# Kernel tuning notes

Hardware: AMD Instinct MI355X
Metric: run time of the kernel (lower is better)

## Reference

```python
import jax, jax.numpy as jnp
import numpy as np

N_EMBD = 1024
N_HEAD = 16
BLOCK_SIZE = 2048
B, T = 4, 2048


def setup_inputs() -> dict:
    key = jax.random.key(0)
    ks = jax.random.split(key, 5)
    x = jax.random.normal(ks[0], (B, T, N_EMBD), dtype=jnp.float32)
    s_in = 1.0 / np.sqrt(N_EMBD)
    W_attn = jax.random.normal(ks[1], (N_EMBD, 3 * N_EMBD), dtype=jnp.float32) * s_in
    b_attn = jnp.zeros((3 * N_EMBD,), dtype=jnp.float32)
    W_proj = jax.random.normal(ks[2], (N_EMBD, N_EMBD), dtype=jnp.float32) * s_in
    b_proj = jnp.zeros((N_EMBD,), dtype=jnp.float32)
    return {"x": x, "W_attn": W_attn, "b_attn": b_attn, "W_proj": W_proj, "b_proj": b_proj}


def reference(x, W_attn, b_attn, W_proj, b_proj):
    Bb, Tt, C = x.shape
    hd = C // N_HEAD  # head_dim = 64
    qkv = x @ W_attn + b_attn                       # [B,T,3C]
    q, k, v = jnp.split(qkv, 3, axis=-1)
    q = q.reshape(Bb, Tt, N_HEAD, hd).transpose(0, 2, 1, 3)  # [B,H,T,hd]
    k = k.reshape(Bb, Tt, N_HEAD, hd).transpose(0, 2, 1, 3)
    v = v.reshape(Bb, Tt, N_HEAD, hd).transpose(0, 2, 1, 3)
    scores = jnp.einsum('bhqd,bhkd->bhqk', q, k) / jnp.sqrt(jnp.float32(hd))
    causal = jnp.tril(jnp.ones((Tt, Tt), dtype=bool))[None, None]
    scores = jnp.where(causal, scores, -jnp.inf)
    attn = jax.nn.softmax(scores, axis=-1)          # [B,H,T,T]
    y = jnp.einsum('bhqk,bhkd->bhqd', attn, v)      # [B,H,T,hd]
    y = y.transpose(0, 2, 1, 3).reshape(Bb, Tt, C)
    return y @ W_proj + b_proj
```

## Files before the change

kernel.cpp:

```cpp
#include <hip/hip_runtime.h>

#define N_EMBD 1024
#define N_HEAD 16
#define HD 64
#define BSZ 4
#define TSEQ 2048
#define MROWS (BSZ * TSEQ)

using bf16x8 = __attribute__((ext_vector_type(8))) short;
using f32x4  = __attribute__((ext_vector_type(4))) float;

__device__ __forceinline__ ushort f2bf(float f) {
    uint u = __float_as_uint(f);
    u += 0x7FFFu + ((u >> 16) & 1u);
    return (ushort)(u >> 16);
}
__device__ __forceinline__ float bf2f(ushort h) {
    return __uint_as_float(((uint)h) << 16);
}

__device__ __forceinline__ void gload16(const ushort* g, short* l) {
    __builtin_amdgcn_global_load_lds(
        (const __attribute__((address_space(1))) void*)g,
        (__attribute__((address_space(3))) void*)l, 16, 0, 0);
}

__global__ __launch_bounds__(256) void split_bf16(const float* __restrict__ A,
                                                  ushort* __restrict__ H,
                                                  ushort* __restrict__ L)
{
    const size_t i = ((size_t)blockIdx.x * 256 + threadIdx.x) * 4;
    const float4 v = *(const float4*)&A[i];
    ushort4 h, l;
    h.x = f2bf(v.x); l.x = f2bf(v.x - bf2f(h.x));
    h.y = f2bf(v.y); l.y = f2bf(v.y - bf2f(h.y));
    h.z = f2bf(v.z); l.z = f2bf(v.z - bf2f(h.z));
    h.w = f2bf(v.w); l.w = f2bf(v.w - bf2f(h.w));
    *(ushort4*)&H[i] = h;
    *(ushort4*)&L[i] = l;
}

__global__ __launch_bounds__(256) void transpose_split(
    const float* __restrict__ W, ushort* __restrict__ Th, ushort* __restrict__ Tl,
    int K, int N)
{
    __shared__ float t[32][33];
    const int k0 = blockIdx.y * 32;
    const int n0 = blockIdx.x * 32;
    const int c = threadIdx.x & 31;
    const int r = threadIdx.x >> 5;
    #pragma unroll
    for (int i = 0; i < 4; ++i)
        t[r + i * 8][c] = W[(size_t)(k0 + r + i * 8) * N + n0 + c];
    __syncthreads();
    #pragma unroll
    for (int i = 0; i < 4; ++i) {
        const float v = t[c][r + i * 8];
        const ushort hb = f2bf(v);
        const ushort lb = f2bf(v - bf2f(hb));
        const size_t o = (size_t)(n0 + r + i * 8) * K + k0 + c;
        Th[o] = hb;
        Tl[o] = lb;
    }
}

__global__ __launch_bounds__(256) void transpose_v(
    const ushort* __restrict__ qkvh, ushort* __restrict__ vth)
{
    __shared__ __align__(16) ushort tr[64][72];
    const int t0 = blockIdx.x * 64;
    const int h  = blockIdx.y;
    const int b  = blockIdx.z;
    const int r  = threadIdx.x >> 2;
    const int c4 = (threadIdx.x & 3) * 16;

    const size_t inb = ((size_t)(b * TSEQ + t0 + r)) * (3 * N_EMBD) + 2 * N_EMBD + h * HD + c4;
    *(float4*)&tr[r][c4]     = *(const float4*)&qkvh[inb];
    *(float4*)&tr[r][c4 + 8] = *(const float4*)&qkvh[inb + 8];
    __syncthreads();

    ushort v[16] __attribute__((aligned(16)));
    #pragma unroll
    for (int u = 0; u < 16; ++u) v[u] = tr[c4 + u][r];
    const size_t ob = (((size_t)(b * N_HEAD + h)) * HD + r) * TSEQ + t0 + c4;
    *(float4*)&vth[ob]     = ((const float4*)v)[0];
    *(float4*)&vth[ob + 8] = ((const float4*)v)[1];
}

template<bool ASPLIT, bool OUTBF16>
__global__ __launch_bounds__(256) void gemm_mfma(
    const ushort* __restrict__ Ah, const ushort* __restrict__ Al,
    const ushort* __restrict__ Bh, const ushort* __restrict__ Bl,
    const float* __restrict__ bias,
    float* __restrict__ Cf, ushort* __restrict__ Ch, ushort* __restrict__ Cl,
    int M, int N, int K)
{
    __shared__ __align__(16) short lds_raw[16384];

    const int tid  = threadIdx.x;
    const int wave = tid >> 6;
    const int lane = tid & 63;
    const int wr   = wave >> 1;
    const int wc   = wave & 1;
    const int row0 = blockIdx.y * 128;
    const int col0 = blockIdx.x * 128;

    const int sr  = wave * 32 + (lane >> 2);
    const int sco = (lane & 3) * 8;
    const ushort* gAh = Ah + (size_t)(row0 + sr) * K + sco;
    const ushort* gAl = ASPLIT ? (Al + (size_t)(row0 + sr) * K + sco) : nullptr;
    const ushort* gBh = Bh + (size_t)(col0 + sr) * K + sco;
    const ushort* gBl = Bl + (size_t)(col0 + sr) * K + sco;
    short* const ldst = lds_raw + wave * 1024;

    const int fr = lane & 15;
    const int fq = lane >> 4;
    const int ko = fq * 8;

    f32x4 acc[4][4] = {};

    for (int k0 = 0; k0 < K; k0 += 32) {
        const size_t K16 = (size_t)16 * K;
        gload16(gAh + k0,       ldst);
        gload16(gAh + k0 + K16, ldst + 512);
        if (ASPLIT) {
            gload16(gAl + k0,       ldst + 4096);
            gload16(gAl + k0 + K16, ldst + 4096 + 512);
        }
        gload16(gBh + k0,       ldst + 8192);
        gload16(gBh + k0 + K16, ldst + 8192 + 512);
        gload16(gBl + k0,       ldst + 12288);
        gload16(gBl + k0 + K16, ldst + 12288 + 512);
        __syncthreads();

        bf16x8 a_h[4], a_l[4], b_h[4], b_l[4];
        #pragma unroll
        for (int m = 0; m < 4; ++m) {
            const int r = wr * 64 + m * 16 + fr;
            a_h[m] = *(const bf16x8*)&lds_raw[r * 32 + ko];
            if (ASPLIT) a_l[m] = *(const bf16x8*)&lds_raw[4096 + r * 32 + ko];
        }
        #pragma unroll
        for (int n = 0; n < 4; ++n) {
            const int r = wc * 64 + n * 16 + fr;
            b_h[n] = *(const bf16x8*)&lds_raw[8192 + r * 32 + ko];
            b_l[n] = *(const bf16x8*)&lds_raw[12288 + r * 32 + ko];
        }

        #pragma unroll
        for (int m = 0; m < 4; ++m)
            #pragma unroll
            for (int n = 0; n < 4; ++n) {
                acc[m][n] = __builtin_amdgcn_mfma_f32_16x16x32_bf16(a_h[m], b_h[n], acc[m][n], 0, 0, 0);
                if (ASPLIT)
                    acc[m][n] = __builtin_amdgcn_mfma_f32_16x16x32_bf16(a_l[m], b_h[n], acc[m][n], 0, 0, 0);
                acc[m][n] = __builtin_amdgcn_mfma_f32_16x16x32_bf16(a_h[m], b_l[n], acc[m][n], 0, 0, 0);
            }
        __syncthreads();
    }

    float bv[4];
    #pragma unroll
    for (int n = 0; n < 4; ++n) bv[n] = bias[col0 + wc * 64 + n * 16 + fr];

    if (OUTBF16) {
        short* wbuf = lds_raw + wave * 2048;
        #pragma unroll
        for (int t = 0; t < 2; ++t) {
            ushort* dst = (t == 0) ? Ch : Cl;
            #pragma unroll
            for (int half = 0; half < 2; ++half) {
                __syncthreads();
                #pragma unroll
                for (int m2 = 0; m2 < 2; ++m2) {
                    const int m = half * 2 + m2;
                    #pragma unroll
                    for (int j = 0; j < 4; ++j)
                        #pragma unroll
                        for (int n = 0; n < 4; ++n) {
                            const float o = acc[m][n][j] + bv[n];
                            const ushort hb = f2bf(o);
                            wbuf[(m2 * 16 + fq * 4 + j) * 64 + n * 16 + fr] =
                                (short)(t == 0 ? hb : f2bf(o - bf2f(hb)));
                        }
                }
                __syncthreads();
                #pragma unroll
                for (int i = 0; i < 4; ++i) {
                    const int r = i * 8 + (lane >> 3);
                    const bf16x8 v = *(const bf16x8*)&wbuf[r * 64 + (lane & 7) * 8];
                    *(bf16x8*)&dst[(size_t)(row0 + wr * 64 + half * 32 + r) * N
                                   + col0 + wc * 64 + (lane & 7) * 8] = v;
                }
            }
        }
    } else {
        float* fbuf = (float*)lds_raw + wave * 2048;
        #pragma unroll
        for (int half = 0; half < 2; ++half) {
            __syncthreads();
            #pragma unroll
            for (int m2 = 0; m2 < 2; ++m2) {
                const int m = half * 2 + m2;
                #pragma unroll
                for (int j = 0; j < 4; ++j)
                    #pragma unroll
                    for (int n = 0; n < 4; ++n)
                        fbuf[(m2 * 16 + fq * 4 + j) * 64 + n * 16 + fr] = acc[m][n][j] + bv[n];
            }
            __syncthreads();
            #pragma unroll
            for (int i = 0; i < 8; ++i) {
                const int r = i * 4 + (lane >> 4);
                const float4 v = *(const float4*)&fbuf[r * 64 + (lane & 15) * 4];
                *(float4*)&Cf[(size_t)(row0 + wr * 64 + half * 32 + r) * N
                              + col0 + wc * 64 + (lane & 15) * 4] = v;
            }
        }
    }
}

__global__ __launch_bounds__(512, 4) void flash_attn_mfma(
    const ushort* __restrict__ qkvh, const ushort* __restrict__ qkvl,
    const ushort* __restrict__ vth, ushort* __restrict__ ath)
{
    __shared__ __align__(16) short Kh[64][64];
    __shared__ __align__(16) short Kl[64][64];
    __shared__ __align__(16) short Vs[64][64];
    __shared__ __align__(16) short Pw[8][2][16][72];

    const int tid  = threadIdx.x;
    const int wave = tid >> 6;
    const int lane = tid & 63;
    const int fr = lane & 15;
    const int g  = lane >> 4;
    const int q0 = blockIdx.x * 128;
    const int h  = blockIdx.y;
    const int b  = blockIdx.z;
    const int qw = q0 + wave * 16;
    const int qg = qw + fr;

    const size_t qrow = ((size_t)(b * TSEQ + qg)) * (3 * N_EMBD) + h * HD + 8 * g;
    const bf16x8 qh0 = *(const bf16x8*)&qkvh[qrow];
    const bf16x8 qh1 = *(const bf16x8*)&qkvh[qrow + 32];
    const bf16x8 ql0 = *(const bf16x8*)&qkvl[qrow];
    const bf16x8 ql1 = *(const bf16x8*)&qkvl[qrow + 32];

    f32x4 O[4] = {};
    float mrun = -1e30f, lrun = 0.f;

    const int sr  = tid >> 3;
    const int su  = tid & 7;
    const int spu = (su ^ (sr & 7)) * 8;
    const int sc  = su * 8;
    const ushort* kgh = qkvh + ((size_t)(b * TSEQ + sr)) * (3 * N_EMBD) + N_EMBD + h * HD + sc;
    const ushort* kgl = qkvl + ((size_t)(b * TSEQ + sr)) * (3 * N_EMBD) + N_EMBD + h * HD + sc;
    const ushort* vg  = vth + (((size_t)(b * N_HEAD + h)) * HD + sr) * TSEQ + sc;

    const int x7  = fr & 7;
    const int ru0 = (g ^ x7) * 8;
    const int ru1 = ((4 + g) ^ x7) * 8;

    const int nt = q0 / 64 + 2;

    float4 nkh = *(const float4*)(kgh);
    float4 nkl = *(const float4*)(kgl);
    float4 nv  = *(const float4*)(vg);

    for (int kt = 0; kt < nt; ++kt) {
        __syncthreads();
        *(float4*)&Kh[sr][spu] = nkh;
        *(float4*)&Kl[sr][spu] = nkl;
        *(float4*)&Vs[sr][spu] = nv;
        __syncthreads();

        if (kt + 1 < nt) {
            nkh = *(const float4*)(kgh + (size_t)(kt + 1) * 64 * 3 * N_EMBD);
            nkl = *(const float4*)(kgl + (size_t)(kt + 1) * 64 * 3 * N_EMBD);
            nv  = *(const float4*)(vg + (kt + 1) * 64);
        }

        if (kt * 64 > qw + 15) continue;

        f32x4 s[4] = {};
        __builtin_amdgcn_s_setprio(1);
        #pragma unroll
        for (int kf = 0; kf < 4; ++kf) {
            const int kr = kf * 16 + fr;
            const bf16x8 kh0 = *(const bf16x8*)&Kh[kr][ru0];
            const bf16x8 kl0 = *(const bf16x8*)&Kl[kr][ru0];
            const bf16x8 kh1 = *(const bf16x8*)&Kh[kr][ru1];
            const bf16x8 kl1 = *(const bf16x8*)&Kl[kr][ru1];
            s[kf] = __builtin_amdgcn_mfma_f32_16x16x32_bf16(kh0, qh0, s[kf], 0, 0, 0);
            s[kf] = __builtin_amdgcn_mfma_f32_16x16x32_bf16(kl0, qh0, s[kf], 0, 0, 0);
            s[kf] = __builtin_amdgcn_mfma_f32_16x16x32_bf16(kh0, ql0, s[kf], 0, 0, 0);
            s[kf] = __builtin_amdgcn_mfma_f32_16x16x32_bf16(kh1, qh1, s[kf], 0, 0, 0);
            s[kf] = __builtin_amdgcn_mfma_f32_16x16x32_bf16(kl1, qh1, s[kf], 0, 0, 0);
            s[kf] = __builtin_amdgcn_mfma_f32_16x16x32_bf16(kh1, ql1, s[kf], 0, 0, 0);
        }
        __builtin_amdgcn_s_setprio(0);

        const bool dm = (kt * 64 + 63 > qw);
        float tmax = -1e30f;
        #pragma unroll
        for (int kf = 0; kf < 4; ++kf)
            #pragma unroll
            for (int j = 0; j < 4; ++j) {
                float v = s[kf][j] * 0.125f;
                if (dm && (kt * 64 + kf * 16 + 4 * g + j > qg)) v = -1e30f;
                s[kf][j] = v;
                tmax = fmaxf(tmax, v);
            }
        tmax = fmaxf(tmax, __shfl_xor(tmax, 16));
        tmax = fmaxf(tmax, __shfl_xor(tmax, 32));
        const float mn = fmaxf(mrun, tmax);
        const float sf = __expf(mrun - mn);
        mrun = mn;
        lrun *= sf;
        #pragma unroll
        for (int df = 0; df < 4; ++df)
            #pragma unroll
            for (int j = 0; j < 4; ++j) O[df][j] *= sf;

        #pragma unroll
        for (int kf = 0; kf < 4; ++kf) {
            uint hw0, hw1, lw0, lw1;
            {
                const float p0 = __expf(s[kf][0] - mn);
                const float p1 = __expf(s[kf][1] - mn);
                const float p2 = __expf(s[kf][2] - mn);
                const float p3 = __expf(s[kf][3] - mn);
                const ushort h0 = f2bf(p0), h1 = f2bf(p1), h2 = f2bf(p2), h3 = f2bf(p3);
                const ushort l0 = f2bf(p0 - bf2f(h0)), l1 = f2bf(p1 - bf2f(h1));
                const ushort l2 = f2bf(p2 - bf2f(h2)), l3 = f2bf(p3 - bf2f(h3));
                lrun += (bf2f(h0) + bf2f(l0)) + (bf2f(h1) + bf2f(l1))
                      + (bf2f(h2) + bf2f(l2)) + (bf2f(h3) + bf2f(l3));
                hw0 = (uint)h0 | ((uint)h1 << 16);
                hw1 = (uint)h2 | ((uint)h3 << 16);
                lw0 = (uint)l0 | ((uint)l1 << 16);
                lw1 = (uint)l2 | ((uint)l3 << 16);
            }
            const int kb = kf * 16 + 4 * g;
            *(uint*)&Pw[wave][0][fr][kb]     = hw0;
            *(uint*)&Pw[wave][0][fr][kb + 2] = hw1;
            *(uint*)&Pw[wave][1][fr][kb]     = lw0;
            *(uint*)&Pw[wave][1][fr][kb + 2] = lw1;
        }

        #pragma unroll
        for (int c = 0; c < 2; ++c) {
            const bf16x8 pbh = *(const bf16x8*)&Pw[wave][0][fr][c * 32 + 8 * g];
            const bf16x8 pbl = *(const bf16x8*)&Pw[wave][1][fr][c * 32 + 8 * g];
            const int rvc = ((4 * c + g) ^ x7) * 8;
            __builtin_amdgcn_s_setprio(1);
            #pragma unroll
            for (int df = 0; df < 4; ++df) {
                const bf16x8 va = *(const bf16x8*)&Vs[df * 16 + fr][rvc];
                O[df] = __builtin_amdgcn_mfma_f32_16x16x32_bf16(va, pbh, O[df], 0, 0, 0);
                O[df] = __builtin_amdgcn_mfma_f32_16x16x32_bf16(va, pbl, O[df], 0, 0, 0);
            }
            __builtin_amdgcn_s_setprio(0);
        }
    }

    lrun += __shfl_xor(lrun, 16);
    lrun += __shfl_xor(lrun, 32);
    const float inv = 1.f / lrun;

    float* Ol = (float*)&Pw[wave][0][0][0];
    #pragma unroll
    for (int df = 0; df < 4; ++df)
        #pragma unroll
        for (int j = 0; j < 4; ++j)
            Ol[fr * 68 + df * 16 + 4 * g + j] = O[df][j] * inv;

    const int q2 = lane >> 2;
    const int dl = (lane & 3) * 4;
    const size_t orow = ((size_t)(b * TSEQ + q0 + wave * 16 + q2)) * N_EMBD + h * HD;
    #pragma unroll
    for (int i = 0; i < 4; ++i) {
        const float4 y = *(const float4*)&Ol[q2 * 68 + dl + 16 * i];
        ushort4 o4;
        o4.x = f2bf(y.x); o4.y = f2bf(y.y); o4.z = f2bf(y.z); o4.w = f2bf(y.w);
        *(ushort4*)&ath[orow + dl + 16 * i] = o4;
    }
}

extern "C" void kernel_launch(void* const* d_in, const int* in_sizes, int n_in,
                              void* d_out, int out_size, void* d_ws, size_t ws_size,
                              hipStream_t stream) {
    const float* x      = (const float*)d_in[0];
    const float* W_attn = (const float*)d_in[1];
    const float* b_attn = (const float*)d_in[2];
    const float* W_proj = (const float*)d_in[3];
    const float* b_proj = (const float*)d_in[4];
    float* out = (float*)d_out;
    (void)in_sizes; (void)n_in; (void)out_size; (void)ws_size;

    char* ws = (char*)d_ws;
    ushort* qkvh = (ushort*)ws; ws += (size_t)MROWS * 3 * N_EMBD * 2;
    ushort* qkvl = (ushort*)ws; ws += (size_t)MROWS * 3 * N_EMBD * 2;
    ushort* xh   = (ushort*)ws; ws += (size_t)MROWS * N_EMBD * 2;
    ushort* xl   = (ushort*)ws; ws += (size_t)MROWS * N_EMBD * 2;
    ushort* wah  = (ushort*)ws; ws += (size_t)3 * N_EMBD * N_EMBD * 2;
    ushort* wal  = (ushort*)ws; ws += (size_t)3 * N_EMBD * N_EMBD * 2;
    ushort* wph  = (ushort*)ws; ws += (size_t)N_EMBD * N_EMBD * 2;
    ushort* wpl  = (ushort*)ws; ws += (size_t)N_EMBD * N_EMBD * 2;
    ushort* vth  = (ushort*)ws; ws += (size_t)MROWS * N_EMBD * 2;
    ushort* ath  = (ushort*)ws;

    dim3 blk(256);

    split_bf16<<<dim3(MROWS * N_EMBD / 1024), blk, 0, stream>>>(x, xh, xl);
    transpose_split<<<dim3(3 * N_EMBD / 32, N_EMBD / 32), blk, 0, stream>>>(
        W_attn, wah, wal, N_EMBD, 3 * N_EMBD);
    transpose_split<<<dim3(N_EMBD / 32, N_EMBD / 32), blk, 0, stream>>>(
        W_proj, wph, wpl, N_EMBD, N_EMBD);

    gemm_mfma<true, true><<<dim3(3 * N_EMBD / 128, MROWS / 128), blk, 0, stream>>>(
        xh, xl, wah, wal, b_attn, nullptr, qkvh, qkvl, MROWS, 3 * N_EMBD, N_EMBD);

    transpose_v<<<dim3(TSEQ / 64, N_HEAD, BSZ), blk, 0, stream>>>(qkvh, vth);

    flash_attn_mfma<<<dim3(TSEQ / 128, N_HEAD, BSZ), dim3(512), 0, stream>>>(
        qkvh, qkvl, vth, ath);

    gemm_mfma<false, false><<<dim3(N_EMBD / 128, MROWS / 128), blk, 0, stream>>>(
        ath, nullptr, wph, wpl, b_proj, out, nullptr, nullptr, MROWS, N_EMBD, N_EMBD);
}
```

Before: 515.8 us.

## Fold softmax scale into Q weights, use exp2, lazy rescale, and swizzle blocks

```diff
diff --git a/kernel.cpp b/kernel.cpp
--- a/kernel.cpp
+++ b/kernel.cpp
@@ -7,6 +7,8 @@
 #define TSEQ 2048
 #define MROWS (BSZ * TSEQ)
 
+#define QSCALE 0.1803368801111204f
+
 using bf16x8 = __attribute__((ext_vector_type(8))) short;
 using f32x4  = __attribute__((ext_vector_type(4))) float;
 
@@ -17,6 +19,13 @@
 }
 __device__ __forceinline__ float bf2f(ushort h) {
     return __uint_as_float(((uint)h) << 16);
+}
+__device__ __forceinline__ float fexp2(float x) {
+#if __has_builtin(__builtin_amdgcn_exp2f)
+    return __builtin_amdgcn_exp2f(x);
+#else
+    return exp2f(x);
+#endif
 }
 
 __device__ __forceinline__ void gload16(const ushort* g, short* l) {
@@ -42,7 +51,7 @@
 
 __global__ __launch_bounds__(256) void transpose_split(
     const float* __restrict__ W, ushort* __restrict__ Th, ushort* __restrict__ Tl,
-    int K, int N)
+    int K, int N, int scaled_rows, float rowscale)
 {
     __shared__ float t[32][33];
     const int k0 = blockIdx.y * 32;
@@ -55,10 +64,12 @@
     __syncthreads();
     #pragma unroll
     for (int i = 0; i < 4; ++i) {
-        const float v = t[c][r + i * 8];
+        const int n = n0 + r + i * 8;
+        float v = t[c][r + i * 8];
+        if (n < scaled_rows) v *= rowscale;
         const ushort hb = f2bf(v);
         const ushort lb = f2bf(v - bf2f(hb));
-        const size_t o = (size_t)(n0 + r + i * 8) * K + k0 + c;
+        const size_t o = (size_t)n * K + k0 + c;
         Th[o] = hb;
         Tl[o] = lb;
     }
@@ -93,17 +104,23 @@
     const ushort* __restrict__ Bh, const ushort* __restrict__ Bl,
     const float* __restrict__ bias,
     float* __restrict__ Cf, ushort* __restrict__ Ch, ushort* __restrict__ Cl,
-    int M, int N, int K)
+    int M, int N, int K, int qcols)
 {
     __shared__ __align__(16) short lds_raw[16384];
+
+    const uint flat = blockIdx.y * gridDim.x + blockIdx.x;
+    const uint nwg  = gridDim.x * gridDim.y;
+    const uint swz  = (flat & 7) * (nwg >> 3) + (flat >> 3);
+    const int  bx   = swz % gridDim.x;
+    const int  by   = swz / gridDim.x;
 
     const int tid  = threadIdx.x;
     const int wave = tid >> 6;
     const int lane = tid & 63;
     const int wr   = wave >> 1;
     const int wc   = wave & 1;
-    const int row0 = blockIdx.y * 128;
-    const int col0 = blockIdx.x * 128;
+    const int row0 = by * 128;
+    const int col0 = bx * 128;
 
     const int sr  = wave * 32 + (lane >> 2);
     const int sco = (lane & 3) * 8;
@@ -161,7 +178,10 @@
 
     float bv[4];
     #pragma unroll
-    for (int n = 0; n < 4; ++n) bv[n] = bias[col0 + wc * 64 + n * 16 + fr];
+    for (int n = 0; n < 4; ++n) {
+        const int cc = col0 + wc * 64 + n * 16 + fr;
+        bv[n] = bias[cc] * (cc < qcols ? QSCALE : 1.f);
+    }
 
     if (OUTBF16) {
         short* wbuf = lds_raw + wave * 2048;
@@ -229,14 +249,17 @@
     __shared__ __align__(16) short Vs[64][64];
     __shared__ __align__(16) short Pw[8][2][16][72];
 
+    const uint flat = blockIdx.x + (blockIdx.y << 4) + (blockIdx.z << 8);
+    const uint swzb = (flat & 7) * 128 + (flat >> 3);
+    const int q0 = (int)(swzb & 15) * 128;
+    const int h  = (int)(swzb >> 4) & 15;
+    const int b  = (int)(swzb >> 8);
+
     const int tid  = threadIdx.x;
     const int wave = tid >> 6;
     const int lane = tid & 63;
     const int fr = lane & 15;
     const int g  = lane >> 4;
-    const int q0 = blockIdx.x * 128;
-    const int h  = blockIdx.y;
-    const int b  = blockIdx.z;
     const int qw = q0 + wave * 16;
     const int qg = qw + fr;
 
@@ -306,40 +329,42 @@
         for (int kf = 0; kf < 4; ++kf)
             #pragma unroll
             for (int j = 0; j < 4; ++j) {
-                float v = s[kf][j] * 0.125f;
+                float v = s[kf][j];
                 if (dm && (kt * 64 + kf * 16 + 4 * g + j > qg)) v = -1e30f;
                 s[kf][j] = v;
                 tmax = fmaxf(tmax, v);
             }
         tmax = fmaxf(tmax, __shfl_xor(tmax, 16));
         tmax = fmaxf(tmax, __shfl_xor(tmax, 32));
-        const float mn = fmaxf(mrun, tmax);
-        const float sf = __expf(mrun - mn);
-        mrun = mn;
-        lrun *= sf;
-        #pragma unroll
-        for (int df = 0; df < 4; ++df)
-            #pragma unroll
-            for (int j = 0; j < 4; ++j) O[df][j] *= sf;
+
+        float mn = mrun;
+        if (!__all(tmax <= mrun + 8.f)) {
+            mn = fmaxf(mrun, tmax);
+            const float sf = fexp2(mrun - mn);
+            mrun = mn;
+            lrun *= sf;
+            #pragma unroll
+            for (int df = 0; df < 4; ++df)
+                #pragma unroll
+                for (int j = 0; j < 4; ++j) O[df][j] *= sf;
+        }
 
         #pragma unroll
         for (int kf = 0; kf < 4; ++kf) {
+            const float p0 = fexp2(s[kf][0] - mn);
+            const float p1 = fexp2(s[kf][1] - mn);
+            const float p2 = fexp2(s[kf][2] - mn);
+            const float p3 = fexp2(s[kf][3] - mn);
+            lrun += (p0 + p1) + (p2 + p3);
             uint hw0, hw1, lw0, lw1;
-            {
-                const float p0 = __expf(s[kf][0] - mn);
-                const float p1 = __expf(s[kf][1] - mn);
-                const float p2 = __expf(s[kf][2] - mn);
-                const float p3 = __expf(s[kf][3] - mn);
-                const ushort h0 = f2bf(p0), h1 = f2bf(p1), h2 = f2bf(p2), h3 = f2bf(p3);
-                const ushort l0 = f2bf(p0 - bf2f(h0)), l1 = f2bf(p1 - bf2f(h1));
-                const ushort l2 = f2bf(p2 - bf2f(h2)), l3 = f2bf(p3 - bf2f(h3));
-                lrun += (bf2f(h0) + bf2f(l0)) + (bf2f(h1) + bf2f(l1))
-                      + (bf2f(h2) + bf2f(l2)) + (bf2f(h3) + bf2f(l3));
-                hw0 = (uint)h0 | ((uint)h1 << 16);
-                hw1 = (uint)h2 | ((uint)h3 << 16);
-                lw0 = (uint)l0 | ((uint)l1 << 16);
-                lw1 = (uint)l2 | ((uint)l3 << 16);
-            }
+            asm("v_cvt_pk_bf16_f32 %0, %1, %2" : "=v"(hw0) : "v"(p0), "v"(p1));
+            asm("v_cvt_pk_bf16_f32 %0, %1, %2" : "=v"(hw1) : "v"(p2), "v"(p3));
+            const float r0 = p0 - __uint_as_float(hw0 << 16);
+            const float r1 = p1 - __uint_as_float(hw0 & 0xFFFF0000u);
+            const float r2 = p2 - __uint_as_float(hw1 << 16);
+            const float r3 = p3 - __uint_as_float(hw1 & 0xFFFF0000u);
+            asm("v_cvt_pk_bf16_f32 %0, %1, %2" : "=v"(lw0) : "v"(r0), "v"(r1));
+            asm("v_cvt_pk_bf16_f32 %0, %1, %2" : "=v"(lw1) : "v"(r2), "v"(r3));
             const int kb = kf * 16 + 4 * g;
             *(uint*)&Pw[wave][0][fr][kb]     = hw0;
             *(uint*)&Pw[wave][0][fr][kb + 2] = hw1;
@@ -413,12 +438,13 @@
 
     split_bf16<<<dim3(MROWS * N_EMBD / 1024), blk, 0, stream>>>(x, xh, xl);
     transpose_split<<<dim3(3 * N_EMBD / 32, N_EMBD / 32), blk, 0, stream>>>(
-        W_attn, wah, wal, N_EMBD, 3 * N_EMBD);
+        W_attn, wah, wal, N_EMBD, 3 * N_EMBD, N_EMBD, QSCALE);
     transpose_split<<<dim3(N_EMBD / 32, N_EMBD / 32), blk, 0, stream>>>(
-        W_proj, wph, wpl, N_EMBD, N_EMBD);
+        W_proj, wph, wpl, N_EMBD, N_EMBD, 0, 1.f);
 
     gemm_mfma<true, true><<<dim3(3 * N_EMBD / 128, MROWS / 128), blk, 0, stream>>>(
-        xh, xl, wah, wal, b_attn, nullptr, qkvh, qkvl, MROWS, 3 * N_EMBD, N_EMBD);
+        xh, xl, wah, wal, b_attn, nullptr, qkvh, qkvl, MROWS, 3 * N_EMBD, N_EMBD,
+        N_EMBD);
 
     transpose_v<<<dim3(TSEQ / 64, N_HEAD, BSZ), blk, 0, stream>>>(qkvh, vth);
 
@@ -426,5 +452,6 @@
         qkvh, qkvl, vth, ath);
 
     gemm_mfma<false, false><<<dim3(N_EMBD / 128, MROWS / 128), blk, 0, stream>>>(
-        ath, nullptr, wph, wpl, b_proj, out, nullptr, nullptr, MROWS, N_EMBD, N_EMBD);
-}
+        ath, nullptr, wph, wpl, b_proj, out, nullptr, nullptr, MROWS, N_EMBD, N_EMBD,
+        0);
+}
```

Result: faster. 465.3 us (-9.8%).
